# Performance work log

Hardware: AMD Instinct MI355X
Metric: run time of the kernel (lower is better)

Reference implementation:

```python
import jax, jax.numpy as jnp
import numpy as np

LAPLACIAN = jnp.array([[-1., -1., -1.], [-1., 8., -1.], [-1., -1., -1.]], dtype=jnp.float32)


def setup_inputs() -> dict:
    key = jax.random.key(0)
    k1, k2 = jax.random.split(key)
    pred = jax.random.normal(k1, (8, 19, 512, 512), dtype=jnp.float32)
    target = jax.random.randint(k2, (8, 512, 512), 0, 19, dtype=jnp.int32)
    return {"pred": pred, "target": target}


def _boundary(x):
    # x: [B, C, H, W] -> abs(clamp(laplacian(x))) per (batch, class) plane
    B, C, H, W = x.shape
    xr = x.reshape(B * C, 1, H, W)
    kern = LAPLACIAN[None, None, :, :]  # [O=1, I=1, 3, 3]
    y = jax.lax.conv_general_dilated(xr, kern, window_strides=(1, 1), padding="SAME")
    return jnp.clip(jnp.abs(y), 0.0, 1.0).reshape(B, C, H, W)


def reference(pred, target):
    # softmax over class dim
    p = jax.nn.softmax(pred, axis=1)
    B, C, H, W = p.shape
    # one-hot target masks: (target[i] == c).float()
    onehot = (target[:, None, :, :] == jnp.arange(C, dtype=target.dtype)[None, :, None, None]).astype(p.dtype)
    pb = _boundary(p)
    tb = _boundary(onehot)
    # sum over (b,c) of per-plane MSE, / (B*C)  == global mean of squared diff
    return jnp.mean((pb - tb) ** 2)
```

## Files before the change

### kernel.cpp

```cpp
#include <hip/hip_runtime.h>

#define NB 8
#define NC 19
#define NH 512
#define NW 512
#define HWP (NH * NW)

#define TW 32
#define TH 16
#define HB_W 40
#define HB_H 18
#define PLANE (HB_W * HB_H)
#define NQ_W 10
#define NQUAD (HB_H * NQ_W)
#define NPAIR 10
#define NTHREADS 256
#define NBLOCKS 4096

typedef _Float16 h2 __attribute__((ext_vector_type(2)));

static __device__ __forceinline__ unsigned int h2_to_u(h2 v) {
    return __builtin_bit_cast(unsigned int, v);
}
static __device__ __forceinline__ h2 u_to_h2(unsigned int u) {
    return __builtin_bit_cast(h2, u);
}

#if __has_builtin(__builtin_amdgcn_cvt_pkrtz)
static __device__ __forceinline__ h2 cvt_pk2(float a, float b) {
    return __builtin_bit_cast(h2, __builtin_amdgcn_cvt_pkrtz(a, b));
}
#else
static __device__ __forceinline__ h2 cvt_pk2(float a, float b) {
    h2 r; r[0] = (_Float16)a; r[1] = (_Float16)b; return r;
}
#endif

#if __has_builtin(__builtin_amdgcn_fdot2)
static __device__ __forceinline__ float fdot2f(h2 a, h2 b, float c) {
    return __builtin_amdgcn_fdot2(a, b, c, false);
}
#else
static __device__ __forceinline__ float fdot2f(h2 a, h2 b, float c) {
    return c + (float)a[0] * (float)b[0] + (float)a[1] * (float)b[1];
}
#endif

__global__ __launch_bounds__(NTHREADS, 5) void bl_main(
    const float* __restrict__ pred, const int* __restrict__ target,
    float* __restrict__ partial)
{
    __shared__ unsigned int e_lds[NPAIR][PLANE];
    __shared__ int t_lds[PLANE];

    const int tid = threadIdx.x;
    const int n = blockIdx.x;
    const int tI = ((n & 7) << 9) + (n >> 3);
    const int bz = tI >> 9;
    const int rem = tI & 511;
    const int by = rem >> 4;
    const int bx = rem & 15;

    const int h0 = by * TH - 1;
    const int gx0 = bx * TW - 4;
    const float* predb = pred + (size_t)bz * NC * HWP;
    const int* tgtb = target + (size_t)bz * HWP;

    if (tid < NQUAD) {
        const int r = tid / NQ_W;
        const int q = tid - r * NQ_W;
        const int gh = h0 + r;
        const int gq = gx0 + (q << 2);
        const int ghc = min(max(gh, 0), NH - 1);
        const int gqc = min(max(gq, 0), NW - 4);
        const bool rowok = (gh >= 0) && (gh < NH);
        const float* src = predb + (size_t)ghc * NW + gqc;

        float4 av[NPAIR];
        float4 bv[NPAIR - 1];
        #pragma unroll
        for (int j = 0; j < NPAIR; ++j)
            av[j] = *reinterpret_cast<const float4*>(
                src + (size_t)(2 * j) * HWP);
        #pragma unroll
        for (int j = 0; j < NPAIR - 1; ++j)
            bv[j] = *reinterpret_cast<const float4*>(
                src + (size_t)(2 * j + 1) * HWP);
        const int4 tv = *reinterpret_cast<const int4*>(
            tgtb + (size_t)ghc * NW + gqc);

        float s0 = 0.f, s1 = 0.f, s2 = 0.f, s3 = 0.f;
        unsigned int pkv[NPAIR][4];

        #pragma unroll
        for (int j = 0; j < NPAIR; ++j) {
            const float ea0 = __expf(av[j].x), ea1 = __expf(av[j].y);
            const float ea2 = __expf(av[j].z), ea3 = __expf(av[j].w);
            float eb0 = 0.f, eb1 = 0.f, eb2 = 0.f, eb3 = 0.f;
            if (j < NPAIR - 1) {
                eb0 = __expf(bv[j].x); eb1 = __expf(bv[j].y);
                eb2 = __expf(bv[j].z); eb3 = __expf(bv[j].w);
            }
            s0 += ea0 + eb0; s1 += ea1 + eb1;
            s2 += ea2 + eb2; s3 += ea3 + eb3;
            pkv[j][0] = h2_to_u(cvt_pk2(ea0, eb0));
            pkv[j][1] = h2_to_u(cvt_pk2(ea1, eb1));
            pkv[j][2] = h2_to_u(cvt_pk2(ea2, eb2));
            pkv[j][3] = h2_to_u(cvt_pk2(ea3, eb3));
        }

        #define NORM_PX(E, SE, OK)                                          \
        {                                                                   \
            const float invf = (OK) ? __builtin_amdgcn_rcpf(SE) : 0.f;      \
            const _Float16 ih = (_Float16)invf;                             \
            h2 ih2v; ih2v[0] = ih; ih2v[1] = ih;                            \
            _Pragma("unroll")                                               \
            for (int j = 0; j < NPAIR; ++j)                                 \
                pkv[j][E] = h2_to_u(u_to_h2(pkv[j][E]) * ih2v);             \
        }
        const bool ok0 = rowok && (gq + 0 >= 0) && (gq + 0 < NW);
        const bool ok1 = rowok && (gq + 1 >= 0) && (gq + 1 < NW);
        const bool ok2 = rowok && (gq + 2 >= 0) && (gq + 2 < NW);
        const bool ok3 = rowok && (gq + 3 >= 0) && (gq + 3 < NW);
        NORM_PX(0, s0, ok0) NORM_PX(1, s1, ok1)
        NORM_PX(2, s2, ok2) NORM_PX(3, s3, ok3)
        #undef NORM_PX

        const int lb = r * HB_W + (q << 2);
        #pragma unroll
        for (int j = 0; j < NPAIR; ++j) {
            *reinterpret_cast<uint4*>(&e_lds[j][lb]) =
                make_uint4(pkv[j][0], pkv[j][1], pkv[j][2], pkv[j][3]);
        }

        int4 tw;
        tw.x = ok0 ? tv.x : 31;
        tw.y = ok1 ? tv.y : 31;
        tw.z = ok2 ? tv.z : 31;
        tw.w = ok3 ? tv.w : 31;
        *reinterpret_cast<int4*>(&t_lds[lb]) = tw;
    }
    __syncthreads();

    float acc = 0.f;
    if (tid >= 128) {
        const int t = tid - 128;
        const int u = t & 15;
        const int s = t >> 4;
        const int r0 = 2 * s;
        const int cw = 2 * u + 2;

        int w[4][4];
        #pragma unroll
        for (int r = 0; r < 4; ++r) {
            const int base = (r0 + r) * HB_W + cw;
            const int2 mdl = *reinterpret_cast<const int2*>(&t_lds[base + 2]);
            w[r][0] = t_lds[base + 1];
            w[r][1] = mdl.x;
            w[r][2] = mdl.y;
            w[r][3] = t_lds[base + 4];
        }

        unsigned int rm[2][4];
        #pragma unroll
        for (int r = 0; r < 4; ++r) {
            const unsigned b1 = 1u << w[r][0];
            const unsigned b2 = 1u << w[r][1];
            const unsigned b3 = 1u << w[r][2];
            const unsigned b4 = 1u << w[r][3];
            const unsigned mm = b2 | b3;
            rm[0][r] = mm | b1;
            rm[1][r] = mm | b4;
        }
        unsigned int mpx[2][2];
        #pragma unroll
        for (int jc = 0; jc < 2; ++jc) {
            const unsigned mid = rm[jc][1] | rm[jc][2];
            #pragma unroll
            for (int k = 0; k < 2; ++k) {
                unsigned m = mid | rm[jc][k ? 3 : 0];
                m = (__popc(m) == 1) ? 0u : (m & 0x7FFFFu);
                mpx[jc][k] = m;
                acc += (float)__popc(m);
            }
        }

        h2 one2;  one2[0] = (_Float16)1.f;  one2[1] = (_Float16)1.f;
        h2 nine2; nine2[0] = (_Float16)9.f; nine2[1] = (_Float16)9.f;

        #pragma unroll
        for (int j = 0; j < NPAIR; ++j) {
            const unsigned int* plane = &e_lds[j][0];
            h2 rs[2][4];
            h2 ctr[2][2];
            #pragma unroll
            for (int r = 0; r < 4; ++r) {
                const int base = (r0 + r) * HB_W + cw;
                const uint2 pm = *reinterpret_cast<const uint2*>(&plane[base + 2]);
                const h2 v1 = u_to_h2(plane[base + 1]);
                const h2 v2 = u_to_h2(pm.x);
                const h2 v3 = u_to_h2(pm.y);
                const h2 v4 = u_to_h2(plane[base + 4]);
                const h2 tm = v2 + v3;
                rs[0][r] = v1 + tm;
                rs[1][r] = tm + v4;
                if (r == 1) { ctr[0][0] = v2; ctr[1][0] = v3; }
                if (r == 2) { ctr[0][1] = v2; ctr[1][1] = v3; }
            }
            #pragma unroll
            for (int jc = 0; jc < 2; ++jc) {
                const h2 midv = rs[jc][1] + rs[jc][2];
                #pragma unroll
                for (int k = 0; k < 2; ++k) {
                    const h2 S = midv + rs[jc][k ? 3 : 0];
                    const h2 lap = ctr[jc][k] * nine2 - S;
                    const h2 ab = u_to_h2(h2_to_u(lap) & 0x7FFF7FFFu);
                    h2 mn;
                    mn[0] = ab[0] < one2[0] ? ab[0] : one2[0];
                    mn[1] = ab[1] < one2[1] ? ab[1] : one2[1];
                    acc = fdot2f(mn, mn, acc);
                    const unsigned bits = (mpx[jc][k] >> (2 * j)) & 3u;
                    const unsigned nt = (bits & 1u ? 0x0000C000u : 0u) |
                                        (bits & 2u ? 0xC0000000u : 0u);
                    acc = fdot2f(mn, u_to_h2(nt), acc);
                }
            }
        }
    }

    #pragma unroll
    for (int off = 32; off > 0; off >>= 1)
        acc += __shfl_down(acc, off, 64);

    __shared__ float wsum[NTHREADS / 64];
    if ((tid & 63) == 0) wsum[tid >> 6] = acc;
    __syncthreads();
    if (tid == 0) {
        float s = 0.f;
        #pragma unroll
        for (int i = 0; i < NTHREADS / 64; ++i) s += wsum[i];
        partial[n] = s;
    }
}

__global__ __launch_bounds__(1024) void bl_reduce(
    const float4* __restrict__ partial, float* __restrict__ out)
{
    const float4 v = partial[threadIdx.x];
    float s = v.x + v.y + v.z + v.w;
    #pragma unroll
    for (int off = 32; off > 0; off >>= 1)
        s += __shfl_down(s, off, 64);
    __shared__ float wsum[16];
    if ((threadIdx.x & 63) == 0) wsum[threadIdx.x >> 6] = s;
    __syncthreads();
    if (threadIdx.x == 0) {
        float t = 0.f;
        #pragma unroll
        for (int i = 0; i < 16; ++i) t += wsum[i];
        out[0] = t * (1.0f / ((float)NB * NC * NH * NW));
    }
}

extern "C" void kernel_launch(void* const* d_in, const int* in_sizes, int n_in,
                              void* d_out, int out_size, void* d_ws, size_t ws_size,
                              hipStream_t stream) {
    const float* pred = (const float*)d_in[0];
    const int* target = (const int*)d_in[1];
    float* partial = (float*)d_ws;

    bl_main<<<dim3(NBLOCKS), NTHREADS, 0, stream>>>(pred, target, partial);
    bl_reduce<<<1, 1024, 0, stream>>>((const float4*)partial, (float*)d_out);
}
```

Before: 37.57 us.

## Halve tile height, double block count, and interleave loads with exp to cut registers

Tile height drops from 16 to 8 rows, which doubles the grid to 8192 blocks. Each compute thread now produces one output row instead of two, and the launch-bounds occupancy hint rises from 5 to 8. The global loads are moved inside the exp loop rather than all issued up front, which lowers register pressure to support the higher occupancy. The cost is more halo overhead (10 staged rows per 8 output rows instead of 18 per 16), less memory-level parallelism per thread, and a larger partial-sum reduction.

```diff
diff --git a/kernel.cpp b/kernel.cpp
--- a/kernel.cpp
+++ b/kernel.cpp
@@ -7,15 +7,15 @@
 #define HWP (NH * NW)
 
 #define TW 32
-#define TH 16
+#define TH 8
 #define HB_W 40
-#define HB_H 18
+#define HB_H 10
 #define PLANE (HB_W * HB_H)
 #define NQ_W 10
 #define NQUAD (HB_H * NQ_W)
 #define NPAIR 10
 #define NTHREADS 256
-#define NBLOCKS 4096
+#define NBLOCKS 8192
 
 typedef _Float16 h2 __attribute__((ext_vector_type(2)));
 
@@ -46,7 +46,7 @@
 }
 #endif
 
-__global__ __launch_bounds__(NTHREADS, 5) void bl_main(
+__global__ __launch_bounds__(NTHREADS, 8) void bl_main(
     const float* __restrict__ pred, const int* __restrict__ target,
     float* __restrict__ partial)
 {
@@ -55,9 +55,9 @@
 
     const int tid = threadIdx.x;
     const int n = blockIdx.x;
-    const int tI = ((n & 7) << 9) + (n >> 3);
-    const int bz = tI >> 9;
-    const int rem = tI & 511;
+    const int tI = ((n & 7) << 10) + (n >> 3);
+    const int bz = tI >> 10;
+    const int rem = tI & 1023;
     const int by = rem >> 4;
     const int bx = rem & 15;
 
@@ -76,16 +76,6 @@
         const bool rowok = (gh >= 0) && (gh < NH);
         const float* src = predb + (size_t)ghc * NW + gqc;
 
-        float4 av[NPAIR];
-        float4 bv[NPAIR - 1];
-        #pragma unroll
-        for (int j = 0; j < NPAIR; ++j)
-            av[j] = *reinterpret_cast<const float4*>(
-                src + (size_t)(2 * j) * HWP);
-        #pragma unroll
-        for (int j = 0; j < NPAIR - 1; ++j)
-            bv[j] = *reinterpret_cast<const float4*>(
-                src + (size_t)(2 * j + 1) * HWP);
         const int4 tv = *reinterpret_cast<const int4*>(
             tgtb + (size_t)ghc * NW + gqc);
 
@@ -94,12 +84,16 @@
 
         #pragma unroll
         for (int j = 0; j < NPAIR; ++j) {
-            const float ea0 = __expf(av[j].x), ea1 = __expf(av[j].y);
-            const float ea2 = __expf(av[j].z), ea3 = __expf(av[j].w);
+            const float4 a = *reinterpret_cast<const float4*>(
+                src + (size_t)(2 * j) * HWP);
+            const float ea0 = __expf(a.x), ea1 = __expf(a.y);
+            const float ea2 = __expf(a.z), ea3 = __expf(a.w);
             float eb0 = 0.f, eb1 = 0.f, eb2 = 0.f, eb3 = 0.f;
             if (j < NPAIR - 1) {
-                eb0 = __expf(bv[j].x); eb1 = __expf(bv[j].y);
-                eb2 = __expf(bv[j].z); eb3 = __expf(bv[j].w);
+                const float4 b = *reinterpret_cast<const float4*>(
+                    src + (size_t)(2 * j + 1) * HWP);
+                eb0 = __expf(b.x); eb1 = __expf(b.y);
+                eb2 = __expf(b.z); eb3 = __expf(b.w);
             }
             s0 += ea0 + eb0; s1 += ea1 + eb1;
             s2 += ea2 + eb2; s3 += ea3 + eb3;
@@ -146,14 +140,13 @@
     if (tid >= 128) {
         const int t = tid - 128;
         const int u = t & 15;
-        const int s = t >> 4;
-        const int r0 = 2 * s;
+        const int row = t >> 4;
         const int cw = 2 * u + 2;
 
-        int w[4][4];
-        #pragma unroll
-        for (int r = 0; r < 4; ++r) {
-            const int base = (r0 + r) * HB_W + cw;
+        int w[3][4];
+        #pragma unroll
+        for (int r = 0; r < 3; ++r) {
+            const int base = (row + r) * HB_W + cw;
             const int2 mdl = *reinterpret_cast<const int2*>(&t_lds[base + 2]);
             w[r][0] = t_lds[base + 1];
             w[r][1] = mdl.x;
@@ -161,26 +154,24 @@
             w[r][3] = t_lds[base + 4];
         }
 
-        unsigned int rm[2][4];
-        #pragma unroll
-        for (int r = 0; r < 4; ++r) {
-            const unsigned b1 = 1u << w[r][0];
-            const unsigned b2 = 1u << w[r][1];
-            const unsigned b3 = 1u << w[r][2];
-            const unsigned b4 = 1u << w[r][3];
-            const unsigned mm = b2 | b3;
-            rm[0][r] = mm | b1;
-            rm[1][r] = mm | b4;
-        }
-        unsigned int mpx[2][2];
-        #pragma unroll
-        for (int jc = 0; jc < 2; ++jc) {
-            const unsigned mid = rm[jc][1] | rm[jc][2];
-            #pragma unroll
-            for (int k = 0; k < 2; ++k) {
-                unsigned m = mid | rm[jc][k ? 3 : 0];
+        unsigned int mpx[2];
+        {
+            unsigned int rm[2][3];
+            #pragma unroll
+            for (int r = 0; r < 3; ++r) {
+                const unsigned b1 = 1u << w[r][0];
+                const unsigned b2 = 1u << w[r][1];
+                const unsigned b3 = 1u << w[r][2];
+                const unsigned b4 = 1u << w[r][3];
+                const unsigned mm = b2 | b3;
+                rm[0][r] = mm | b1;
+                rm[1][r] = mm | b4;
+            }
+            #pragma unroll
+            for (int jc = 0; jc < 2; ++jc) {
+                unsigned m = rm[jc][0] | rm[jc][1] | rm[jc][2];
                 m = (__popc(m) == 1) ? 0u : (m & 0x7FFFFu);
-                mpx[jc][k] = m;
+                mpx[jc] = m;
                 acc += (float)__popc(m);
             }
         }
@@ -191,11 +182,11 @@
         #pragma unroll
         for (int j = 0; j < NPAIR; ++j) {
             const unsigned int* plane = &e_lds[j][0];
-            h2 rs[2][4];
-            h2 ctr[2][2];
-            #pragma unroll
-            for (int r = 0; r < 4; ++r) {
-                const int base = (r0 + r) * HB_W + cw;
+            h2 rs[2][3];
+            h2 ctr[2];
+            #pragma unroll
+            for (int r = 0; r < 3; ++r) {
+                const int base = (row + r) * HB_W + cw;
                 const uint2 pm = *reinterpret_cast<const uint2*>(&plane[base + 2]);
                 const h2 v1 = u_to_h2(plane[base + 1]);
                 const h2 v2 = u_to_h2(pm.x);
@@ -204,26 +195,21 @@
                 const h2 tm = v2 + v3;
                 rs[0][r] = v1 + tm;
                 rs[1][r] = tm + v4;
-                if (r == 1) { ctr[0][0] = v2; ctr[1][0] = v3; }
-                if (r == 2) { ctr[0][1] = v2; ctr[1][1] = v3; }
+                if (r == 1) { ctr[0] = v2; ctr[1] = v3; }
             }
             #pragma unroll
             for (int jc = 0; jc < 2; ++jc) {
-                const h2 midv = rs[jc][1] + rs[jc][2];
-                #pragma unroll
-                for (int k = 0; k < 2; ++k) {
-                    const h2 S = midv + rs[jc][k ? 3 : 0];
-                    const h2 lap = ctr[jc][k] * nine2 - S;
-                    const h2 ab = u_to_h2(h2_to_u(lap) & 0x7FFF7FFFu);
-                    h2 mn;
-                    mn[0] = ab[0] < one2[0] ? ab[0] : one2[0];
-                    mn[1] = ab[1] < one2[1] ? ab[1] : one2[1];
-                    acc = fdot2f(mn, mn, acc);
-                    const unsigned bits = (mpx[jc][k] >> (2 * j)) & 3u;
-                    const unsigned nt = (bits & 1u ? 0x0000C000u : 0u) |
-                                        (bits & 2u ? 0xC0000000u : 0u);
-                    acc = fdot2f(mn, u_to_h2(nt), acc);
-                }
+                const h2 S = rs[jc][0] + rs[jc][1] + rs[jc][2];
+                const h2 lap = ctr[jc] * nine2 - S;
+                const h2 ab = u_to_h2(h2_to_u(lap) & 0x7FFF7FFFu);
+                h2 mn;
+                mn[0] = ab[0] < one2[0] ? ab[0] : one2[0];
+                mn[1] = ab[1] < one2[1] ? ab[1] : one2[1];
+                acc = fdot2f(mn, mn, acc);
+                const unsigned bits = (mpx[jc] >> (2 * j)) & 3u;
+                const unsigned nt = (bits & 1u ? 0x0000C000u : 0u) |
+                                    (bits & 2u ? 0xC0000000u : 0u);
+                acc = fdot2f(mn, u_to_h2(nt), acc);
             }
         }
     }
@@ -246,8 +232,9 @@
 __global__ __launch_bounds__(1024) void bl_reduce(
     const float4* __restrict__ partial, float* __restrict__ out)
 {
-    const float4 v = partial[threadIdx.x];
-    float s = v.x + v.y + v.z + v.w;
+    const float4 v0 = partial[threadIdx.x];
+    const float4 v1 = partial[threadIdx.x + 1024];
+    float s = (v0.x + v0.y + v0.z + v0.w) + (v1.x + v1.y + v1.z + v1.w);
     #pragma unroll
     for (int off = 32; off > 0; off >>= 1)
         s += __shfl_down(s, off, 64);
```

After: 59.60 us. 58.6% more time.
